# Performance work log

Hardware: AMD Instinct MI355X
Metric: run time of the kernel (lower is better)

## Reference

```python
import jax, jax.numpy as jnp
import numpy as np

E = 262144
D = 128          # node/edge latent dim
H = 512          # MLP hidden dim
IN = 3 * D       # concat of x_i, x_j, edge_attr
LN_EPS = 1e-5


def setup_inputs() -> dict:
    key = jax.random.key(0)
    ks = jax.random.split(key, 9)
    s1 = 1.0 / np.sqrt(IN)
    s2 = 1.0 / np.sqrt(H)
    return {
        "x_i": jax.random.normal(ks[0], (E, D), dtype=jnp.float32),
        "x_j": jax.random.normal(ks[1], (E, D), dtype=jnp.float32),
        "edge_attr": jax.random.normal(ks[2], (E, D), dtype=jnp.float32),
        "W1": jax.random.uniform(ks[3], (IN, H), jnp.float32, -s1, s1),
        "b1": jax.random.uniform(ks[4], (H,), jnp.float32, -s1, s1),
        "W2": jax.random.uniform(ks[5], (H, D), jnp.float32, -s2, s2),
        "b2": jax.random.uniform(ks[6], (D,), jnp.float32, -s2, s2),
        "gamma": jnp.ones((D,), dtype=jnp.float32),
        "beta": jnp.zeros((D,), dtype=jnp.float32),
    }


def reference(x_i, x_j, edge_attr, W1, b1, W2, b2, gamma, beta):
    # concat -> Linear -> SiLU -> Linear -> LayerNorm -> +edge_attr (residual)
    h = jnp.concatenate([x_i, x_j, edge_attr], axis=-1)        # [E, 3D]
    h = jax.nn.silu(h @ W1 + b1)                                # [E, H]
    h = h @ W2 + b2                                             # [E, D]
    mu = jnp.mean(h, axis=-1, keepdims=True)
    var = jnp.mean(jnp.square(h - mu), axis=-1, keepdims=True)
    h = (h - mu) * jax.lax.rsqrt(var + LN_EPS) * gamma + beta   # LayerNorm
    return h + edge_attr
```

## Files before the change

kernel.cpp:

```cpp
#include <hip/hip_runtime.h>
#include <hip/hip_bf16.h>

typedef __bf16 bf16;
typedef __attribute__((ext_vector_type(8))) __bf16 bf16x8;
typedef __attribute__((ext_vector_type(4))) float f32x4;

#define E_EDGES 262144
#define MT 128

__global__ void transpose_w(const float* __restrict__ W1, const float* __restrict__ W2,
                            bf16* __restrict__ W1t, bf16* __restrict__ W2t)
{
  int tid = blockIdx.x * 256 + threadIdx.x;
  if (tid < 512 * 384) {
    int n = tid / 384;
    int k = tid - n * 384;
    W1t[tid] = (bf16)W1[k * 512 + n];
  }
  if (tid < 128 * 512) {
    int n = tid >> 9;
    int k = tid & 511;
    W2t[tid] = (bf16)W2[k * 128 + n];
  }
}

__device__ __forceinline__ bf16x8 cvt8(const float* p) {
  f32x4 a = *(const f32x4*)p;
  f32x4 b = *(const f32x4*)(p + 4);
  bf16x8 r;
  r[0] = (bf16)a[0]; r[1] = (bf16)a[1]; r[2] = (bf16)a[2]; r[3] = (bf16)a[3];
  r[4] = (bf16)b[0]; r[5] = (bf16)b[1]; r[6] = (bf16)b[2]; r[7] = (bf16)b[3];
  return r;
}

__global__ __launch_bounds__(512, 4)
void fused_edge_mlp(const float* __restrict__ x_i,
                    const float* __restrict__ x_j,
                    const float* __restrict__ ea,
                    const bf16* __restrict__ W1t,
                    const float* __restrict__ b1,
                    const bf16* __restrict__ W2t,
                    const float* __restrict__ b2,
                    const float* __restrict__ gmm,
                    const float* __restrict__ bta,
                    float* __restrict__ out)
{
  __shared__ bf16 As[128 * 32];
  __shared__ bf16 Bs[128 * 32];
  __shared__ bf16 W2s[128 * 32];
  __shared__ bf16 H1s[128 * 136];

  const int t    = threadIdx.x;
  const int w    = t >> 6;
  const int lane = t & 63;
  const int l15  = lane & 15;
  const int q    = lane >> 4;
  const int srow = t >> 2;
  const int sc8  = (t & 3) << 3;
  const int wm   = w >> 2;
  const int wn   = w & 3;
  const long m0  = (long)blockIdx.x * MT;

  const f32x4 fzero = {0.f, 0.f, 0.f, 0.f};

  f32x4 acc2[8];
  #pragma unroll
  for (int i = 0; i < 8; ++i) acc2[i] = fzero;

  for (int nc = 0; nc < 4; ++nc) {
    f32x4 acc1[8];
    #pragma unroll
    for (int i = 0; i < 8; ++i) acc1[i] = fzero;

    for (int kk = 0; kk < 12; ++kk) {
      const float* src = (kk < 4) ? x_i : (kk < 8) ? x_j : ea;
      bf16x8 av = cvt8(src + (m0 + srow) * 128 + ((kk & 3) << 5) + sc8);
      bf16x8 bv = *(const bf16x8*)(W1t + (long)(nc * 128 + srow) * 384 + (kk << 5) + sc8);

      __syncthreads();
      *(bf16x8*)&As[srow * 32 + sc8] = av;
      *(bf16x8*)&Bs[srow * 32 + sc8] = bv;
      __syncthreads();

      bf16x8 af[4], bfr[2];
      #pragma unroll
      for (int mi = 0; mi < 4; ++mi)
        af[mi] = *(const bf16x8*)&As[(64 * wm + 16 * mi + l15) * 32 + 8 * q];
      #pragma unroll
      for (int ni = 0; ni < 2; ++ni)
        bfr[ni] = *(const bf16x8*)&Bs[(32 * wn + 16 * ni + l15) * 32 + 8 * q];
      #pragma unroll
      for (int mi = 0; mi < 4; ++mi)
        #pragma unroll
        for (int ni = 0; ni < 2; ++ni)
          acc1[mi * 2 + ni] = __builtin_amdgcn_mfma_f32_16x16x32_bf16(
              af[mi], bfr[ni], acc1[mi * 2 + ni], 0, 0, 0);
    }

    {
      float b1v[2];
      #pragma unroll
      for (int ni = 0; ni < 2; ++ni)
        b1v[ni] = b1[nc * 128 + 32 * wn + 16 * ni + l15];
      #pragma unroll
      for (int mi = 0; mi < 4; ++mi)
        #pragma unroll
        for (int ni = 0; ni < 2; ++ni)
          #pragma unroll
          for (int i = 0; i < 4; ++i) {
            float s = acc1[mi * 2 + ni][i] + b1v[ni];
            float h = s / (1.f + __expf(-s));
            H1s[(64 * wm + 16 * mi + 4 * q + i) * 136 + 32 * wn + 16 * ni + l15] = (bf16)h;
          }
    }

    for (int s4 = 0; s4 < 4; ++s4) {
      bf16x8 wv = *(const bf16x8*)(W2t + (long)srow * 512 + nc * 128 + (s4 << 5) + sc8);

      __syncthreads();
      *(bf16x8*)&W2s[srow * 32 + sc8] = wv;
      __syncthreads();

      bf16x8 a2 = *(const bf16x8*)&H1s[(16 * w + l15) * 136 + (s4 << 5) + 8 * q];
      #pragma unroll
      for (int ni = 0; ni < 8; ++ni) {
        bf16x8 b2f = *(const bf16x8*)&W2s[(16 * ni + l15) * 32 + 8 * q];
        acc2[ni] = __builtin_amdgcn_mfma_f32_16x16x32_bf16(a2, b2f, acc2[ni], 0, 0, 0);
      }
    }
  }

  float b2v[8], gv[8], bv[8];
  #pragma unroll
  for (int ni = 0; ni < 8; ++ni) {
    int n = 16 * ni + l15;
    b2v[ni] = b2[n];
    gv[ni]  = gmm[n];
    bv[ni]  = bta[n];
  }
  #pragma unroll
  for (int ni = 0; ni < 8; ++ni)
    #pragma unroll
    for (int i = 0; i < 4; ++i)
      acc2[ni][i] += b2v[ni];

  #pragma unroll
  for (int i = 0; i < 4; ++i) {
    float s = 0.f, s2 = 0.f;
    #pragma unroll
    for (int ni = 0; ni < 8; ++ni) {
      float v = acc2[ni][i];
      s += v;
      s2 += v * v;
    }
    #pragma unroll
    for (int off = 1; off <= 8; off <<= 1) {
      s  += __shfl_xor(s,  off, 64);
      s2 += __shfl_xor(s2, off, 64);
    }
    float mu   = s * (1.f / 128.f);
    float var  = fmaxf(s2 * (1.f / 128.f) - mu * mu, 0.f);
    float rstd = rsqrtf(var + 1e-5f);
    long  mg   = m0 + 16 * w + 4 * q + i;
    #pragma unroll
    for (int ni = 0; ni < 8; ++ni) {
      int n = 16 * ni + l15;
      float o = (acc2[ni][i] - mu) * rstd * gv[ni] + bv[ni] + ea[mg * 128 + n];
      out[mg * 128 + n] = o;
    }
  }
}

extern "C" void kernel_launch(void* const* d_in, const int* in_sizes, int n_in,
                              void* d_out, int out_size, void* d_ws, size_t ws_size,
                              hipStream_t stream)
{
  const float* x_i = (const float*)d_in[0];
  const float* x_j = (const float*)d_in[1];
  const float* ea  = (const float*)d_in[2];
  const float* W1  = (const float*)d_in[3];
  const float* b1  = (const float*)d_in[4];
  const float* W2  = (const float*)d_in[5];
  const float* b2  = (const float*)d_in[6];
  const float* gm  = (const float*)d_in[7];
  const float* bt  = (const float*)d_in[8];
  float* outp = (float*)d_out;
  bf16* W1t = (bf16*)d_ws;
  bf16* W2t = W1t + 512 * 384;

  hipLaunchKernelGGL(transpose_w, dim3(768), dim3(256), 0, stream, W1, W2, W1t, W2t);
  hipLaunchKernelGGL(fused_edge_mlp, dim3(E_EDGES / MT), dim3(512), 0, stream,
                     x_i, x_j, ea, W1t, b1, W2t, b2, gm, bt, outp);
}
```

Measured before the change: 628.4 us.

## Double-buffer LDS tiles with direct global-to-LDS loads and XOR swizzle

Converts the main GEMM loops to a double-buffered software pipeline. The next A tile is loaded into registers and the next weight tile is issued with global_load_lds into the alternate buffer while MFMAs run on the current one, which leaves one barrier per step instead of two. Shared memory tiles use an XOR swizzle to cut bank conflicts, W2 tiles reuse the A buffer, and b1 is hoisted into registers. This adds complexity in buffer indexing and relies on global_load_lds completing before the barrier. LDS usage rises, which may limit occupancy.

```diff
diff --git a/kernel.cpp b/kernel.cpp
--- a/kernel.cpp
+++ b/kernel.cpp
@@ -24,13 +24,18 @@
   }
 }
 
-__device__ __forceinline__ bf16x8 cvt8(const float* p) {
-  f32x4 a = *(const f32x4*)p;
-  f32x4 b = *(const f32x4*)(p + 4);
+__device__ __forceinline__ bf16x8 cvt8v(f32x4 a, f32x4 b) {
   bf16x8 r;
   r[0] = (bf16)a[0]; r[1] = (bf16)a[1]; r[2] = (bf16)a[2]; r[3] = (bf16)a[3];
   r[4] = (bf16)b[0]; r[5] = (bf16)b[1]; r[6] = (bf16)b[2]; r[7] = (bf16)b[3];
   return r;
+}
+
+__device__ __forceinline__ void glds16(const void* g, void* l) {
+  __builtin_amdgcn_global_load_lds(
+      (const __attribute__((address_space(1))) void*)g,
+      (__attribute__((address_space(3))) void*)l,
+      16, 0, 0);
 }
 
 __global__ __launch_bounds__(512, 4)
@@ -45,9 +50,8 @@
                     const float* __restrict__ bta,
                     float* __restrict__ out)
 {
-  __shared__ bf16 As[128 * 32];
-  __shared__ bf16 Bs[128 * 32];
-  __shared__ bf16 W2s[128 * 32];
+  __shared__ bf16 As[2][128 * 32];
+  __shared__ bf16 Bs[2][128 * 32];
   __shared__ bf16 H1s[128 * 136];
 
   const int t    = threadIdx.x;
@@ -56,77 +60,110 @@
   const int l15  = lane & 15;
   const int q    = lane >> 4;
   const int srow = t >> 2;
-  const int sc8  = (t & 3) << 3;
+  const int sc   = t & 3;
+  const int scf  = sc << 3;
+  const int swz  = (sc ^ ((srow >> 1) & 3)) << 3;
+  const int rsw  = (l15 >> 1) & 3;
   const int wm   = w >> 2;
   const int wn   = w & 3;
   const long m0  = (long)blockIdx.x * MT;
+  const int wb   = (t & ~63) << 3;
 
   const f32x4 fzero = {0.f, 0.f, 0.f, 0.f};
 
+  float b1r[8];
+  #pragma unroll
+  for (int j = 0; j < 8; ++j)
+    b1r[j] = b1[(j >> 1) * 128 + 32 * wn + 16 * (j & 1) + l15];
+
   f32x4 acc2[8];
   #pragma unroll
   for (int i = 0; i < 8; ++i) acc2[i] = fzero;
 
+  {
+    const float* pA = x_i + (m0 + srow) * 128 + scf;
+    f32x4 a0 = *(const f32x4*)pA;
+    f32x4 a1 = *(const f32x4*)(pA + 4);
+    glds16(W1t + (long)srow * 384 + swz, &Bs[0][wb]);
+    *(bf16x8*)&As[0][srow * 32 + swz] = cvt8v(a0, a1);
+    __syncthreads();
+  }
+
+  int p = 0;
   for (int nc = 0; nc < 4; ++nc) {
     f32x4 acc1[8];
     #pragma unroll
     for (int i = 0; i < 8; ++i) acc1[i] = fzero;
 
     for (int kk = 0; kk < 12; ++kk) {
-      const float* src = (kk < 4) ? x_i : (kk < 8) ? x_j : ea;
-      bf16x8 av = cvt8(src + (m0 + srow) * 128 + ((kk & 3) << 5) + sc8);
-      bf16x8 bv = *(const bf16x8*)(W1t + (long)(nc * 128 + srow) * 384 + (kk << 5) + sc8);
-
-      __syncthreads();
-      *(bf16x8*)&As[srow * 32 + sc8] = av;
-      *(bf16x8*)&Bs[srow * 32 + sc8] = bv;
-      __syncthreads();
+      f32x4 a0, a1;
+      if (kk < 11) {
+        const int k1 = kk + 1;
+        const float* sA = (k1 < 4) ? x_i : (k1 < 8) ? x_j : ea;
+        const float* pA = sA + (m0 + srow) * 128 + ((k1 & 3) << 5) + scf;
+        a0 = *(const f32x4*)pA;
+        a1 = *(const f32x4*)(pA + 4);
+        glds16(W1t + (long)(nc * 128 + srow) * 384 + (k1 << 5) + swz, &Bs[p ^ 1][wb]);
+      } else {
+        glds16(W2t + (long)srow * 512 + (nc << 7) + swz, &As[p ^ 1][wb]);
+      }
 
       bf16x8 af[4], bfr[2];
       #pragma unroll
       for (int mi = 0; mi < 4; ++mi)
-        af[mi] = *(const bf16x8*)&As[(64 * wm + 16 * mi + l15) * 32 + 8 * q];
+        af[mi] = *(const bf16x8*)&As[p][(64 * wm + 16 * mi + l15) * 32 + ((q ^ rsw) << 3)];
       #pragma unroll
       for (int ni = 0; ni < 2; ++ni)
-        bfr[ni] = *(const bf16x8*)&Bs[(32 * wn + 16 * ni + l15) * 32 + 8 * q];
+        bfr[ni] = *(const bf16x8*)&Bs[p][(32 * wn + 16 * ni + l15) * 32 + ((q ^ rsw) << 3)];
       #pragma unroll
       for (int mi = 0; mi < 4; ++mi)
         #pragma unroll
         for (int ni = 0; ni < 2; ++ni)
           acc1[mi * 2 + ni] = __builtin_amdgcn_mfma_f32_16x16x32_bf16(
               af[mi], bfr[ni], acc1[mi * 2 + ni], 0, 0, 0);
-    }
-
-    {
-      float b1v[2];
-      #pragma unroll
-      for (int ni = 0; ni < 2; ++ni)
-        b1v[ni] = b1[nc * 128 + 32 * wn + 16 * ni + l15];
-      #pragma unroll
-      for (int mi = 0; mi < 4; ++mi)
+
+      if (kk < 11) {
+        *(bf16x8*)&As[p ^ 1][srow * 32 + swz] = cvt8v(a0, a1);
+      } else {
         #pragma unroll
-        for (int ni = 0; ni < 2; ++ni)
+        for (int mi = 0; mi < 4; ++mi)
           #pragma unroll
-          for (int i = 0; i < 4; ++i) {
-            float s = acc1[mi * 2 + ni][i] + b1v[ni];
-            float h = s / (1.f + __expf(-s));
-            H1s[(64 * wm + 16 * mi + 4 * q + i) * 136 + 32 * wn + 16 * ni + l15] = (bf16)h;
-          }
+          for (int ni = 0; ni < 2; ++ni)
+            #pragma unroll
+            for (int i = 0; i < 4; ++i) {
+              float s = acc1[mi * 2 + ni][i] + b1r[(nc << 1) + ni];
+              float h = s / (1.f + __expf(-s));
+              H1s[(64 * wm + 16 * mi + 4 * q + i) * 136 + 32 * wn + 16 * ni + l15] = (bf16)h;
+            }
+      }
+      __syncthreads();
+      p ^= 1;
     }
 
     for (int s4 = 0; s4 < 4; ++s4) {
-      bf16x8 wv = *(const bf16x8*)(W2t + (long)srow * 512 + nc * 128 + (s4 << 5) + sc8);
-
+      f32x4 a0, a1;
+      bool stA = false;
+      if (s4 < 3) {
+        glds16(W2t + (long)srow * 512 + (nc << 7) + ((s4 + 1) << 5) + swz, &As[p ^ 1][wb]);
+      } else if (nc < 3) {
+        glds16(W1t + (long)((nc + 1) * 128 + srow) * 384 + swz, &Bs[p ^ 1][wb]);
+        const float* pA = x_i + (m0 + srow) * 128 + scf;
+        a0 = *(const f32x4*)pA;
+        a1 = *(const f32x4*)(pA + 4);
+        stA = true;
+      }
+
+      bf16x8 a2 = *(const bf16x8*)&H1s[(16 * w + l15) * 136 + (s4 << 5) + (q << 3)];
+      #pragma unroll
+      for (int ni = 0; ni < 8; ++ni) {
+        bf16x8 b2f = *(const bf16x8*)&As[p][(16 * ni + l15) * 32 + ((q ^ rsw) << 3)];
+        acc2[ni] = __builtin_amdgcn_mfma_f32_16x16x32_bf16(a2, b2f, acc2[ni], 0, 0, 0);
+      }
+
+      if (stA)
+        *(bf16x8*)&As[p ^ 1][srow * 32 + swz] = cvt8v(a0, a1);
       __syncthreads();
-      *(bf16x8*)&W2s[srow * 32 + sc8] = wv;
-      __syncthreads();
-
-      bf16x8 a2 = *(const bf16x8*)&H1s[(16 * w + l15) * 136 + (s4 << 5) + 8 * q];
-      #pragma unroll
-      for (int ni = 0; ni < 8; ++ni) {
-        bf16x8 b2f = *(const bf16x8*)&W2s[(16 * ni + l15) * 32 + 8 * q];
-        acc2[ni] = __builtin_amdgcn_mfma_f32_16x16x32_bf16(a2, b2f, acc2[ni], 0, 0, 0);
-      }
+      p ^= 1;
     }
   }
 
```

Result: no change. 636.2 us (+1.2%).

## Load MFMA operands directly from global memory, dropping LDS staging for GEMM1 and W2

Applied to the files above, without the earlier changes.

The shared-memory staging of the A tile, the W1 tile and the W2 tile is removed. Each wave now loads its MFMA fragments straight from global memory: fp32 activations are converted to bf16 in registers, and the bf16 weights are read from L2. This removes the two block-wide barriers per k-step and the LDS round trip. In exchange, activation rows are re-read by the four wn waves sharing them, and weight fragments use strided global loads, which raises L2/global traffic and latency exposure.

```diff
diff --git a/kernel.cpp b/kernel.cpp
--- a/kernel.cpp
+++ b/kernel.cpp
@@ -24,9 +24,7 @@
   }
 }
 
-__device__ __forceinline__ bf16x8 cvt8(const float* p) {
-  f32x4 a = *(const f32x4*)p;
-  f32x4 b = *(const f32x4*)(p + 4);
+__device__ __forceinline__ bf16x8 cvt8v(f32x4 a, f32x4 b) {
   bf16x8 r;
   r[0] = (bf16)a[0]; r[1] = (bf16)a[1]; r[2] = (bf16)a[2]; r[3] = (bf16)a[3];
   r[4] = (bf16)b[0]; r[5] = (bf16)b[1]; r[6] = (bf16)b[2]; r[7] = (bf16)b[3];
@@ -45,9 +43,6 @@
                     const float* __restrict__ bta,
                     float* __restrict__ out)
 {
-  __shared__ bf16 As[128 * 32];
-  __shared__ bf16 Bs[128 * 32];
-  __shared__ bf16 W2s[128 * 32];
   __shared__ bf16 H1s[128 * 136];
 
   const int t    = threadIdx.x;
@@ -55,8 +50,6 @@
   const int lane = t & 63;
   const int l15  = lane & 15;
   const int q    = lane >> 4;
-  const int srow = t >> 2;
-  const int sc8  = (t & 3) << 3;
   const int wm   = w >> 2;
   const int wn   = w & 3;
   const long m0  = (long)blockIdx.x * MT;
@@ -67,34 +60,46 @@
   #pragma unroll
   for (int i = 0; i < 8; ++i) acc2[i] = fzero;
 
+  const long aoff = (m0 + 64 * wm + l15) * 128 + 8 * q;
+  const long boff = (long)(32 * wn + l15) * 384 + 8 * q;
+
   for (int nc = 0; nc < 4; ++nc) {
     f32x4 acc1[8];
     #pragma unroll
     for (int i = 0; i < 8; ++i) acc1[i] = fzero;
 
-    for (int kk = 0; kk < 12; ++kk) {
-      const float* src = (kk < 4) ? x_i : (kk < 8) ? x_j : ea;
-      bf16x8 av = cvt8(src + (m0 + srow) * 128 + ((kk & 3) << 5) + sc8);
-      bf16x8 bv = *(const bf16x8*)(W1t + (long)(nc * 128 + srow) * 384 + (kk << 5) + sc8);
+    const bf16* Wb = W1t + (long)nc * 128 * 384 + boff;
 
-      __syncthreads();
-      *(bf16x8*)&As[srow * 32 + sc8] = av;
-      *(bf16x8*)&Bs[srow * 32 + sc8] = bv;
-      __syncthreads();
-
-      bf16x8 af[4], bfr[2];
+    for (int ph = 0; ph < 3; ++ph) {
+      const float* src = (ph == 0) ? x_i : (ph == 1) ? x_j : ea;
+      const float* Ab  = src + aoff;
       #pragma unroll
-      for (int mi = 0; mi < 4; ++mi)
-        af[mi] = *(const bf16x8*)&As[(64 * wm + 16 * mi + l15) * 32 + 8 * q];
-      #pragma unroll
-      for (int ni = 0; ni < 2; ++ni)
-        bfr[ni] = *(const bf16x8*)&Bs[(32 * wn + 16 * ni + l15) * 32 + 8 * q];
-      #pragma unroll
-      for (int mi = 0; mi < 4; ++mi)
+      for (int k4 = 0; k4 < 4; ++k4) {
+        const int kk = ph * 4 + k4;
+        f32x4 a0[4], a1[4];
+        #pragma unroll
+        for (int mi = 0; mi < 4; ++mi) {
+          const float* p = Ab + (long)mi * 16 * 128 + k4 * 32;
+          a0[mi] = *(const f32x4*)p;
+          a1[mi] = *(const f32x4*)(p + 4);
+        }
+        bf16x8 bfr[2];
         #pragma unroll
         for (int ni = 0; ni < 2; ++ni)
-          acc1[mi * 2 + ni] = __builtin_amdgcn_mfma_f32_16x16x32_bf16(
-              af[mi], bfr[ni], acc1[mi * 2 + ni], 0, 0, 0);
+          bfr[ni] = *(const bf16x8*)(Wb + (long)ni * 16 * 384 + kk * 32);
+
+        bf16x8 af[4];
+        #pragma unroll
+        for (int mi = 0; mi < 4; ++mi)
+          af[mi] = cvt8v(a0[mi], a1[mi]);
+
+        #pragma unroll
+        for (int mi = 0; mi < 4; ++mi)
+          #pragma unroll
+          for (int ni = 0; ni < 2; ++ni)
+            acc1[mi * 2 + ni] = __builtin_amdgcn_mfma_f32_16x16x32_bf16(
+                af[mi], bfr[ni], acc1[mi * 2 + ni], 0, 0, 0);
+      }
     }
 
     {
@@ -113,21 +118,19 @@
             H1s[(64 * wm + 16 * mi + 4 * q + i) * 136 + 32 * wn + 16 * ni + l15] = (bf16)h;
           }
     }
+    __syncthreads();
 
+    const bf16* W2b = W2t + nc * 128 + (long)l15 * 512 + 8 * q;
+    #pragma unroll
     for (int s4 = 0; s4 < 4; ++s4) {
-      bf16x8 wv = *(const bf16x8*)(W2t + (long)srow * 512 + nc * 128 + (s4 << 5) + sc8);
-
-      __syncthreads();
-      *(bf16x8*)&W2s[srow * 32 + sc8] = wv;
-      __syncthreads();
-
-      bf16x8 a2 = *(const bf16x8*)&H1s[(16 * w + l15) * 136 + (s4 << 5) + 8 * q];
+      bf16x8 a2 = *(const bf16x8*)&H1s[(16 * w + l15) * 136 + (s4 << 5) + (q << 3)];
       #pragma unroll
       for (int ni = 0; ni < 8; ++ni) {
-        bf16x8 b2f = *(const bf16x8*)&W2s[(16 * ni + l15) * 32 + 8 * q];
+        bf16x8 b2f = *(const bf16x8*)(W2b + (long)ni * 16 * 512 + s4 * 32);
         acc2[ni] = __builtin_amdgcn_mfma_f32_16x16x32_bf16(a2, b2f, acc2[ni], 0, 0, 0);
       }
     }
+    __syncthreads();
   }
 
   float b2v[8], gv[8], bv[8];
```

Result: slower. 1.390 ms (+121.2%).
